# Kernel optimization log

Hardware: AMD Instinct MI355X
Metric: run time of the kernel (lower is better)

## Reference

```python
import jax, jax.numpy as jnp
import numpy as np

N_NODES = 2048
N_EDGES = 32768
DIM = 256
HEADS = 4

PARAM_SHAPES = {
    'Wq': (DIM, DIM), 'bq': (DIM,), 'Wk': (DIM, DIM), 'bk': (DIM,),
    'Wv': (DIM, DIM), 'bv': (DIM,), 'Wo': (DIM, DIM), 'bo': (DIM,),
    'gd_W1': (4, 3), 'gd_b1': (3,), 'gd_W2': (3, HEADS), 'gd_b2': (HEADS,),
    'tw_W1': (2 * DIM, DIM), 'tw_b1': (DIM,), 'tw_W2': (DIM, DIM), 'tw_b2': (DIM,),
    'ne_W1': (4 * DIM, 2 * DIM), 'ne_b1': (2 * DIM,), 'ne_W2': (2 * DIM, DIM), 'ne_b2': (DIM,),
    'att_W1': (2 * DIM // HEADS, 2 * DIM // HEADS), 'att_b1': (2 * DIM // HEADS,),
    'att_W2': (DIM // HEADS, 2 * DIM // HEADS), 'att_b2': (DIM // HEADS,),
    'pe_W': (DIM, DIM), 'pe_b': (DIM,), 'pq_W': (DIM, DIM), 'pq_b': (DIM,),
    'pv_W': (DIM, DIM), 'pv_b': (DIM,),
    'pr_W1': (2 * DIM, 2 * DIM), 'pr_b1': (2 * DIM,), 'pr_W2': (2 * DIM, DIM), 'pr_b2': (DIM,),
}


def _lin(x, W, b):
    return x @ W + b


def _mlp2(x, W1, b1, W2, b2):  # Linear-ReLU-Linear (build_mlp, on_last=False)
    return _lin(jnp.maximum(_lin(x, W1, b1), 0.0), W2, b2)


def setup_inputs() -> dict:
    key = jax.random.key(0)
    ks = iter(jax.random.split(key, 64))
    rng = np.random.default_rng(0)
    half = N_EDGES // 2
    s = rng.integers(0, N_NODES, half)
    d = rng.integers(0, N_NODES, half)
    # reciprocal edge pairs so the reverse-edge lookup path is exercised
    edge_index = jnp.asarray(np.stack([np.concatenate([s, d]), np.concatenate([d, s])]), dtype=jnp.int32)
    inp = {
        'node_f': jax.random.normal(next(ks), (N_NODES, DIM), jnp.float32),
        'edge_f': jax.random.normal(next(ks), (N_EDGES, DIM), jnp.float32),
        'coords': jax.random.normal(next(ks), (N_NODES, 3), jnp.float32),
        'edge_index': edge_index,
        'num_heads': HEADS,
    }
    for name, shp in PARAM_SHAPES.items():
        inp[name] = jax.random.normal(next(ks), shp, jnp.float32) * 0.02
    return inp


def _forward(node_f, edge_f, coords, edge_index, num_heads,
             Wq, bq, Wk, bk, Wv, bv, Wo, bo,
             gd_W1, gd_b1, gd_W2, gd_b2,
             tw_W1, tw_b1, tw_W2, tw_b2,
             ne_W1, ne_b1, ne_W2, ne_b2,
             att_W1, att_b1, att_W2, att_b2,
             pe_W, pe_b, pq_W, pq_b, pv_W, pv_b,
             pr_W1, pr_b1, pr_W2, pr_b2):
    N, Dn = node_f.shape
    E, De = edge_f.shape
    H = num_heads
    dh = Wq.shape[1] // H
    src, dst = edge_index[0], edge_index[1]

    # --- NodeUpdate: distance-aware MHSA over all node pairs (batch=1) ---
    q = _lin(node_f, Wq, bq).reshape(N, H, dh)
    k = _lin(node_f, Wk, bk).reshape(N, H, dh)
    v = _lin(node_f, Wv, bv).reshape(N, H, dh)
    diff = coords[:, None, :] - coords[None, :, :]  # [N,N,3]
    sq = jnp.sum(diff * diff, axis=-1, keepdims=True)
    dist = jnp.where(sq > 0, jnp.sqrt(jnp.where(sq > 0, sq, 1.0)), 0.0)
    dmask = _mlp2(jnp.concatenate([diff, dist], -1), gd_W1, gd_b1, gd_W2, gd_b2)  # [N,N,H]
    scores = jnp.einsum('nhd,mhd->hnm', q, k) / float(dh) ** 0.5 + dmask.transpose(2, 0, 1)
    attn = jax.nn.softmax(scores, axis=-1)
    mhsa = _lin(jnp.einsum('hnm,mhd->nhd', attn, v).reshape(N, H * dh), Wo, bo)

    # --- TwinningEdgeAttention: per-node mean of outgoing / incoming edge feats ---
    ones = jnp.ones((E,), edge_f.dtype)
    cnt_s = jnp.maximum(jax.ops.segment_sum(ones, src, num_segments=N), 1.0)
    cnt_d = jnp.maximum(jax.ops.segment_sum(ones, dst, num_segments=N), 1.0)
    sub_mean = jax.ops.segment_sum(edge_f, src, num_segments=N) / cnt_s[:, None]
    obj_mean = jax.ops.segment_sum(edge_f, dst, num_segments=N) / cnt_d[:, None]
    edge_att = jax.nn.sigmoid(_mlp2(jnp.concatenate([sub_mean, obj_mean], -1), tw_W1, tw_b1, tw_W2, tw_b2))
    node_out = jnp.maximum(mhsa, 0.0) * edge_att  # [N, Dn]

    # --- GraphEdgeAttenNetwork ---
    x_i = node_f[src]
    x_j = node_f[dst]
    # reverse-edge matching (vectorized replacement of the python double loop)
    table = jnp.zeros((N * N,), jnp.int32).at[src * N + dst].set(jnp.arange(E, dtype=jnp.int32) + 1)
    rev = table[dst * N + src]
    rev_feat = jnp.where((rev > 0)[:, None], edge_f[jnp.maximum(rev - 1, 0)], 0.0)
    edge_out = _mlp2(jnp.concatenate([x_i, edge_f, rev_feat, x_j], -1), ne_W1, ne_b1, ne_W2, ne_b2)

    value = _lin(x_j, pv_W, pv_b)  # [E, Da]
    query = _lin(x_i, pq_W, pq_b).reshape(E, Dn // H, H)
    edgep = _lin(edge_f, pe_W, pe_b).reshape(E, De // H, H)
    qe = jnp.concatenate([query, edgep], axis=1)  # [E, d_n+d_e, H]
    # conv1d(kernel=1) MLP over channel axis, ReLU between layers
    h = jnp.maximum(jnp.einsum('ech,oc->eoh', qe, att_W1) + att_b1[None, :, None], 0.0)
    prob = jax.nn.softmax(jnp.einsum('ech,oc->eoh', h, att_W2) + att_b2[None, :, None], axis=1)  # [E, d_o, H]
    msg = prob.reshape(E, -1) * value
    agg = jax.ops.segment_max(msg, src, num_segments=N)
    agg = jnp.where(jnp.isfinite(agg), agg, 0.0)  # empty segments -> 0 (torch scatter_max fill)
    xx = _mlp2(jnp.concatenate([node_f, agg], -1), pr_W1, pr_b1, pr_W2, pr_b2)
    return node_out, edge_out, xx


def reference(node_f, edge_f, coords, edge_index, num_heads,
              Wq, bq, Wk, bk, Wv, bv, Wo, bo,
              gd_W1, gd_b1, gd_W2, gd_b2,
              tw_W1, tw_b1, tw_W2, tw_b2,
              ne_W1, ne_b1, ne_W2, ne_b2,
              att_W1, att_b1, att_W2, att_b2,
              pe_W, pe_b, pq_W, pq_b, pv_W, pv_b,
              pr_W1, pr_b1, pr_W2, pr_b2):
    return _forward(node_f, edge_f, coords, edge_index, num_heads,
                    Wq, bq, Wk, bk, Wv, bv, Wo, bo,
                    gd_W1, gd_b1, gd_W2, gd_b2,
                    tw_W1, tw_b1, tw_W2, tw_b2,
                    ne_W1, ne_b1, ne_W2, ne_b2,
                    att_W1, att_b1, att_W2, att_b2,
                    pe_W, pe_b, pq_W, pq_b, pv_W, pv_b,
                    pr_W1, pr_b1, pr_W2, pr_b2)
```

## Files before the change

### kernel.cpp

```cpp
#include <hip/hip_runtime.h>

#define NN 2048
#define NE 32768
#define DIM 256
#define NH 4

typedef unsigned short u16;
typedef __attribute__((ext_vector_type(4))) unsigned short u16x4;
typedef __attribute__((ext_vector_type(8))) short bf16x8;
typedef __attribute__((ext_vector_type(4))) float f32x4;

typedef __attribute__((address_space(1))) const unsigned int g_as1;
typedef __attribute__((address_space(3))) unsigned int l_as3;

__device__ __forceinline__ void gload16(const u16* g, u16* l) {
  __builtin_amdgcn_global_load_lds((g_as1*)g, (l_as3*)l, 16, 0, 0);
}

__device__ __forceinline__ u16 f2bf(float f) {
  unsigned u = __float_as_uint(f);
  unsigned r = u + 0x7FFFu + ((u >> 16) & 1u);
  return (u16)(r >> 16);
}
__device__ __forceinline__ float bf2f(u16 b) {
  return __uint_as_float(((unsigned)b) << 16);
}

struct GB { const u16* A; const int* idx; long ld; long aoffz; };

template<int BNF, int EPI>
__global__ __launch_bounds__(256) void gemm_bf(
    GB ga, const u16* __restrict__ Bt, long bld, long boffz,
    const float* __restrict__ bias, void* __restrict__ Cp, long ldc, long coffz,
    int K, float scale)
{
  __shared__ u16 As[128 * 64];
  __shared__ u16 Bs[32 * BNF * 64];

  const int tid = threadIdx.x;
  const int wid = tid >> 6, lane = tid & 63;
  const int bz = blockIdx.z;
  const int m0 = blockIdx.y * 128;
  const int n0 = blockIdx.x * (32 * BNF);
  const int wr = wid >> 1, wc = wid & 1;
  const int l15 = lane & 15, l4 = lane >> 4;

  const u16* asrc[4];
  #pragma unroll
  for (int c = 0; c < 4; ++c) {
    int rl = c*32 + wid*8 + (lane >> 3);
    int row = ga.idx ? ga.idx[m0 + rl] : (m0 + rl);
    int c16s = (lane & 7) ^ (rl & 7);
    asrc[c] = ga.A + ga.aoffz * bz + (long)row * ga.ld + c16s * 8;
  }
  const u16* bsrc[BNF];
  #pragma unroll
  for (int c = 0; c < BNF; ++c) {
    int rl = c*32 + wid*8 + (lane >> 3);
    int c16s = (lane & 7) ^ (rl & 7);
    bsrc[c] = Bt + boffz * bz + (long)(n0 + rl) * bld + c16s * 8;
  }

  f32x4 acc[4][BNF] = {};

  for (int k0 = 0; k0 < K; k0 += 64) {
    #pragma unroll
    for (int c = 0; c < 4; ++c)
      gload16(asrc[c] + k0, &As[(c*32 + wid*8) * 64]);
    #pragma unroll
    for (int c = 0; c < BNF; ++c)
      gload16(bsrc[c] + k0, &Bs[(c*32 + wid*8) * 64]);
    __syncthreads();

    #pragma unroll
    for (int kk = 0; kk < 2; ++kk) {
      bf16x8 af[4], bfr[BNF];
      #pragma unroll
      for (int i = 0; i < 4; ++i) {
        int r = wr*64 + i*16 + l15;
        af[i] = *(const bf16x8*)&As[r*64 + (((kk*4 + l4) ^ (r & 7)) * 8)];
      }
      #pragma unroll
      for (int j = 0; j < BNF; ++j) {
        int r = wc*(16*BNF) + j*16 + l15;
        bfr[j] = *(const bf16x8*)&Bs[r*64 + (((kk*4 + l4) ^ (r & 7)) * 8)];
      }
      #pragma unroll
      for (int i = 0; i < 4; ++i)
        #pragma unroll
        for (int j = 0; j < BNF; ++j)
          acc[i][j] = __builtin_amdgcn_mfma_f32_16x16x32_bf16(af[i], bfr[j], acc[i][j], 0, 0, 0);
    }
    __syncthreads();
  }

  #pragma unroll
  for (int j = 0; j < BNF; ++j) {
    const int col = n0 + wc*(16*BNF) + j*16 + l15;
    const float bb = bias ? bias[col] : 0.f;
    #pragma unroll
    for (int i = 0; i < 4; ++i) {
      #pragma unroll
      for (int r = 0; r < 4; ++r) {
        const int m = m0 + wr*64 + i*16 + l4*4 + r;
        float v = acc[i][j][r] * scale + bb;
        if constexpr (EPI == 1) v = fmaxf(v, 0.f);
        if constexpr (EPI == 2) v = 1.f / (1.f + expf(-v));
        if constexpr (EPI == 0 || EPI == 2)
          ((float*)Cp)[coffz*bz + (long)m*ldc + col] = v;
        else if constexpr (EPI == 4)
          ((u16*)Cp)[((long)(col & 3) * NE + m) * ldc + (col >> 2) + coffz] = f2bf(v);
        else if constexpr (EPI == 6)
          ((float*)Cp)[(long)m*256 + (col & 3)*64 + (col >> 2)] = v;
        else if constexpr (EPI == 7)
          ((u16*)Cp)[((long)(col & 3) * NN + m) * ldc + (col >> 2) + coffz] = f2bf(v);
        else
          ((u16*)Cp)[coffz*bz + (long)m*ldc + col] = f2bf(v);
      }
    }
  }
}

__global__ __launch_bounds__(256) void flash_k(
    const u16* __restrict__ qkv,
    const u16* __restrict__ vT,
    const float4* __restrict__ pk,
    const float* __restrict__ gW1, const float* __restrict__ gb1,
    const float* __restrict__ gW2, const float* __restrict__ gb2,
    float* __restrict__ Op,
    float2* __restrict__ ml)
{
  __shared__ u16 Qls[64*64];
  __shared__ u16 Kls[128*64];
  __shared__ u16 Vls[2][64*64];
  __shared__ u16 Pls[4][16*128];

  const int tid = threadIdx.x, wid = tid >> 6, lane = tid & 63;
  const int h  = blockIdx.x & 3;
  const int m0 = (blockIdx.x >> 2) * 64;
  const int part = blockIdx.y;
  const int l15 = lane & 15, l4 = lane >> 4;
  const int rl8 = wid*8 + (lane >> 3);
  const int c8  = lane & 7;

  #pragma unroll
  for (int c = 0; c < 2; ++c) {
    int r = c*32 + rl8;
    gload16(qkv + (long)(m0 + r)*768 + h*64 + ((c8 ^ (r & 7))*8), &Qls[(c*32 + wid*8)*64]);
  }
  __syncthreads();
  bf16x8 qf[2];
  {
    int r = wid*16 + l15;
    qf[0] = *(const bf16x8*)&Qls[r*64 + (((0*4 + l4) ^ (r & 7))*8)];
    qf[1] = *(const bf16x8*)&Qls[r*64 + (((1*4 + l4) ^ (r & 7))*8)];
  }

  const float b10 = gb1[0], b11 = gb1[1], b12 = gb1[2];
  const float w30 = gW1[9], w31 = gW1[10], w32 = gW1[11];
  const float w20 = gW2[0*4+h], w21 = gW2[1*4+h], w22 = gW2[2*4+h];
  const float b2h = gb2[h];
  float4 rp0[4], rp1[4];
  #pragma unroll
  for (int r = 0; r < 4; ++r) {
    int qrow = m0 + wid*16 + l4*4 + r;
    rp0[r] = pk[qrow*2]; rp1[r] = pk[qrow*2 + 1];
  }

  float mrun[4] = {-1e30f, -1e30f, -1e30f, -1e30f};
  float lrun[4] = {};
  f32x4 pa[4] = {};

  for (int t = 0; t < 4; ++t) {
    const int n0 = part*512 + t*128;
    #pragma unroll
    for (int c = 0; c < 4; ++c) {
      int r = c*32 + rl8;
      gload16(qkv + (long)(n0 + r)*768 + 256 + h*64 + ((c8 ^ (r & 7))*8),
              &Kls[(c*32 + wid*8)*64]);
    }
    #pragma unroll
    for (int hh = 0; hh < 2; ++hh)
      #pragma unroll
      for (int c = 0; c < 2; ++c) {
        int r = c*32 + rl8;
        gload16(vT + (long)(h*64 + r)*NN + n0 + hh*64 + ((c8 ^ (r & 7))*8),
                &Vls[hh][(c*32 + wid*8)*64]);
      }
    __syncthreads();

    f32x4 sa[8] = {};
    #pragma unroll
    for (int kk = 0; kk < 2; ++kk) {
      #pragma unroll
      for (int j = 0; j < 8; ++j) {
        int r = j*16 + l15;
        bf16x8 bf = *(const bf16x8*)&Kls[r*64 + (((kk*4 + l4) ^ (r & 7))*8)];
        sa[j] = __builtin_amdgcn_mfma_f32_16x16x32_bf16(qf[kk], bf, sa[j], 0, 0, 0);
      }
    }

    float rowmx[4] = {-1e30f, -1e30f, -1e30f, -1e30f};
    #pragma unroll
    for (int j = 0; j < 8; ++j) {
      int n = n0 + j*16 + l15;
      float4 cp0 = pk[n*2], cp1 = pk[n*2 + 1];
      #pragma unroll
      for (int r = 0; r < 4; ++r) {
        float dot = rp0[r].x*cp0.x + rp0[r].y*cp0.y + rp0[r].z*cp0.z;
        float sq = rp0[r].w + cp0.w - 2.f*dot;
        float dist = sq > 0.f ? sq * __frsqrt_rn(sq) : 0.f;
        float h0 = fmaxf(b10 + rp1[r].x - cp1.x + dist*w30, 0.f);
        float h1 = fmaxf(b11 + rp1[r].y - cp1.y + dist*w31, 0.f);
        float h2 = fmaxf(b12 + rp1[r].z - cp1.z + dist*w32, 0.f);
        float s = sa[j][r]*0.125f + b2h + h0*w20 + h1*w21 + h2*w22;
        sa[j][r] = s;
        rowmx[r] = fmaxf(rowmx[r], s);
      }
    }
    #pragma unroll
    for (int w = 1; w < 16; w <<= 1)
      #pragma unroll
      for (int r = 0; r < 4; ++r)
        rowmx[r] = fmaxf(rowmx[r], __shfl_xor(rowmx[r], w));

    float fac[4], rs[4] = {};
    #pragma unroll
    for (int r = 0; r < 4; ++r) {
      float mnew = fmaxf(mrun[r], rowmx[r]);
      fac[r] = __expf(mrun[r] - mnew);
      mrun[r] = mnew;
    }
    #pragma unroll
    for (int j = 0; j < 8; ++j)
      #pragma unroll
      for (int r = 0; r < 4; ++r) {
        float p = __expf(sa[j][r] - mrun[r]);
        sa[j][r] = p;
        rs[r] += p;
      }
    #pragma unroll
    for (int w = 1; w < 16; w <<= 1)
      #pragma unroll
      for (int r = 0; r < 4; ++r)
        rs[r] += __shfl_xor(rs[r], w);
    #pragma unroll
    for (int r = 0; r < 4; ++r) lrun[r] = lrun[r]*fac[r] + rs[r];
    #pragma unroll
    for (int j2 = 0; j2 < 4; ++j2)
      #pragma unroll
      for (int r = 0; r < 4; ++r)
        pa[j2][r] *= fac[r];

    #pragma unroll
    for (int j = 0; j < 8; ++j)
      #pragma unroll
      for (int r = 0; r < 4; ++r) {
        int qr = l4*4 + r, n = j*16 + l15;
        Pls[wid][qr*128 + (((n >> 3) ^ (qr & 7))*8) + (n & 7)] = f2bf(sa[j][r]);
      }
    #pragma unroll
    for (int ks = 0; ks < 4; ++ks) {
      bf16x8 paf = *(const bf16x8*)&Pls[wid][l15*128 + (((ks*4 + l4) ^ (l15 & 7))*8)];
      #pragma unroll
      for (int j2 = 0; j2 < 4; ++j2) {
        int r = j2*16 + l15;
        bf16x8 vf = *(const bf16x8*)&Vls[ks >> 1][r*64 + ((((ks & 1)*4 + l4) ^ (r & 7))*8)];
        pa[j2] = __builtin_amdgcn_mfma_f32_16x16x32_bf16(paf, vf, pa[j2], 0, 0, 0);
      }
    }
    __syncthreads();
  }

  #pragma unroll
  for (int j2 = 0; j2 < 4; ++j2)
    #pragma unroll
    for (int r = 0; r < 4; ++r) {
      int m = m0 + wid*16 + l4*4 + r;
      Op[((long)part*NN + m)*256 + h*64 + j2*16 + l15] = pa[j2][r];
    }
  if (l15 == 0) {
    #pragma unroll
    for (int r = 0; r < 4; ++r) {
      int m = m0 + wid*16 + l4*4 + r;
      ml[((long)part*NN + m)*4 + h] = make_float2(mrun[r], lrun[r]);
    }
  }
}

__global__ __launch_bounds__(256) void comb_k(const float* __restrict__ Op,
    const float2* __restrict__ ml, u16* __restrict__ attn) {
  int n = blockIdx.x, t = threadIdx.x, h = t >> 6;
  float m[4], l[4];
  #pragma unroll
  for (int p = 0; p < 4; ++p) { float2 v = ml[((long)p*NN + n)*4 + h]; m[p] = v.x; l[p] = v.y; }
  float M = fmaxf(fmaxf(m[0], m[1]), fmaxf(m[2], m[3]));
  float L = 0.f, o = 0.f;
  #pragma unroll
  for (int p = 0; p < 4; ++p) {
    float w = __expf(m[p] - M);
    L += w * l[p];
    o += w * Op[((long)p*NN + n)*256 + t];
  }
  attn[(long)n*256 + t] = f2bf(o / L);
}

__global__ __launch_bounds__(64) void attedge_k(
    const u16* __restrict__ qN, const u16* __restrict__ ep,
    const float* __restrict__ valNp, const int* __restrict__ ei,
    const u16* __restrict__ W1, const float* __restrict__ b1,
    const u16* __restrict__ W2, const float* __restrict__ b2,
    float* __restrict__ msgP)
{
  __shared__ u16 As[32*128];
  const int lane = threadIdx.x;
  const int h = blockIdx.y;
  const int e0 = blockIdx.x * 32;
  const int l15 = lane & 15, l4 = lane >> 4;

  #pragma unroll
  for (int p = 0; p < 8; ++p) {
    int R0 = p*4;
    int r  = R0 + (lane >> 4);
    int cd = lane & 15;
    int cs = ((cd & 7) ^ (r & 7)) | (cd & 8);
    const u16* src = (cs < 8)
        ? qN + ((long)h*NN + ei[e0 + r])*64 + cs*8
        : ep + ((long)h*NE + e0 + r)*64 + (cs & 7)*8;
    gload16(src, &As[R0*128]);
  }
  __syncthreads();

  f32x4 acc1[2][8] = {};
  #pragma unroll
  for (int kk = 0; kk < 4; ++kk) {
    bf16x8 af[2], bfr[8];
    #pragma unroll
    for (int i = 0; i < 2; ++i) {
      int rA = i*16 + l15;
      int cg = kk*4 + l4;
      int cd = ((cg & 7) ^ (rA & 7)) | (cg & 8);
      af[i] = *(const bf16x8*)&As[rA*128 + cd*8];
    }
    #pragma unroll
    for (int j = 0; j < 8; ++j)
      bfr[j] = *(const bf16x8*)&W1[(long)(j*16 + l15)*128 + kk*32 + l4*8];
    #pragma unroll
    for (int i = 0; i < 2; ++i)
      #pragma unroll
      for (int j = 0; j < 8; ++j)
        acc1[i][j] = __builtin_amdgcn_mfma_f32_16x16x32_bf16(af[i], bfr[j], acc1[i][j], 0, 0, 0);
  }
  __syncthreads();
  #pragma unroll
  for (int i = 0; i < 2; ++i)
    #pragma unroll
    for (int j = 0; j < 8; ++j) {
      int n = j*16 + l15;
      float bb = b1[n];
      #pragma unroll
      for (int r = 0; r < 4; ++r) {
        int m = i*16 + l4*4 + r;
        int cg = n >> 3;
        int cd = ((cg & 7) ^ (m & 7)) | (cg & 8);
        As[m*128 + cd*8 + (n & 7)] = f2bf(fmaxf(acc1[i][j][r] + bb, 0.f));
      }
    }
  __syncthreads();

  f32x4 acc2[2][4] = {};
  #pragma unroll
  for (int kk = 0; kk < 4; ++kk) {
    bf16x8 af[2], bfr[4];
    #pragma unroll
    for (int i = 0; i < 2; ++i) {
      int rA = i*16 + l15;
      int cg = kk*4 + l4;
      int cd = ((cg & 7) ^ (rA & 7)) | (cg & 8);
      af[i] = *(const bf16x8*)&As[rA*128 + cd*8];
    }
    #pragma unroll
    for (int j = 0; j < 4; ++j)
      bfr[j] = *(const bf16x8*)&W2[(long)(j*16 + l15)*128 + kk*32 + l4*8];
    #pragma unroll
    for (int i = 0; i < 2; ++i)
      #pragma unroll
      for (int j = 0; j < 4; ++j)
        acc2[i][j] = __builtin_amdgcn_mfma_f32_16x16x32_bf16(af[i], bfr[j], acc2[i][j], 0, 0, 0);
  }

  #pragma unroll
  for (int i = 0; i < 2; ++i) {
    float mx[4] = {-1e30f,-1e30f,-1e30f,-1e30f};
    #pragma unroll
    for (int j = 0; j < 4; ++j) {
      float bb = b2[j*16 + l15];
      #pragma unroll
      for (int r = 0; r < 4; ++r) {
        acc2[i][j][r] += bb;
        mx[r] = fmaxf(mx[r], acc2[i][j][r]);
      }
    }
    #pragma unroll
    for (int w = 1; w < 16; w <<= 1)
      #pragma unroll
      for (int r = 0; r < 4; ++r) mx[r] = fmaxf(mx[r], __shfl_xor(mx[r], w));
    float sum[4] = {};
    #pragma unroll
    for (int j = 0; j < 4; ++j)
      #pragma unroll
      for (int r = 0; r < 4; ++r) {
        float p = __expf(acc2[i][j][r] - mx[r]);
        acc2[i][j][r] = p; sum[r] += p;
      }
    #pragma unroll
    for (int w = 1; w < 16; w <<= 1)
      #pragma unroll
      for (int r = 0; r < 4; ++r) sum[r] += __shfl_xor(sum[r], w);
    #pragma unroll
    for (int r = 0; r < 4; ++r) {
      int m = i*16 + l4*4 + r;
      int e = e0 + m;
      int dst = ei[NE + e];
      float inv = 1.f / sum[r];
      #pragma unroll
      for (int j = 0; j < 4; ++j) {
        int o = j*16 + l15;
        float v = valNp[(long)dst*256 + h*64 + o];
        msgP[(long)e*256 + h*64 + o] = acc2[i][j][r] * inv * v;
      }
    }
  }
}

__global__ __launch_bounds__(256) void gemm_ne(
    const u16* __restrict__ nbf, const u16* __restrict__ ebf, const u16* __restrict__ zbuf,
    const int* __restrict__ ei, const int* __restrict__ rev,
    const u16* __restrict__ Bt, const float* __restrict__ bias, u16* __restrict__ C)
{
  __shared__ u16 As[128 * 64];
  __shared__ u16 Bs[128 * 64];
  const int tid = threadIdx.x, wid = tid >> 6, lane = tid & 63;
  const int lin = blockIdx.y * 4 + blockIdx.x;
  const int xcd = lin & 7, seq = lin >> 3;
  const int m0 = (xcd*32 + (seq >> 2)) * 128;
  const int n0 = (seq & 3) * 128;
  const int wr = wid >> 1, wc = wid & 1, l15 = lane & 15, l4 = lane >> 4;

  const u16* bsrc[4];
  #pragma unroll
  for (int c = 0; c < 4; ++c) {
    int rl = c*32 + wid*8 + (lane >> 3);
    int c16s = (lane & 7) ^ (rl & 7);
    bsrc[c] = Bt + (long)(n0 + rl) * 1024 + c16s * 8;
  }

  f32x4 acc[4][4] = {};

  #pragma unroll
  for (int seg = 0; seg < 4; ++seg) {
    const u16* asrc[4];
    #pragma unroll
    for (int c = 0; c < 4; ++c) {
      int rl = c*32 + wid*8 + (lane >> 3);
      int m = m0 + rl;
      int c16s = (lane & 7) ^ (rl & 7);
      const u16* base; long row;
      if (seg == 0)      { base = nbf; row = ei[m]; }
      else if (seg == 1) { base = ebf; row = m; }
      else if (seg == 2) { int r = rev[m]; base = (r >= 0) ? ebf : zbuf; row = (r >= 0) ? r : 0; }
      else               { base = nbf; row = ei[NE + m]; }
      asrc[c] = base + row * 256 + c16s * 8;
    }
    #pragma unroll
    for (int kt = 0; kt < 4; ++kt) {
      #pragma unroll
      for (int c = 0; c < 4; ++c)
        gload16(asrc[c] + kt*64, &As[(c*32 + wid*8) * 64]);
      #pragma unroll
      for (int c = 0; c < 4; ++c)
        gload16(bsrc[c] + seg*256 + kt*64, &Bs[(c*32 + wid*8) * 64]);
      __syncthreads();
      #pragma unroll
      for (int kk = 0; kk < 2; ++kk) {
        bf16x8 af[4], bfr[4];
        #pragma unroll
        for (int i = 0; i < 4; ++i) {
          int r = wr*64 + i*16 + l15;
          af[i] = *(const bf16x8*)&As[r*64 + (((kk*4 + l4) ^ (r & 7)) * 8)];
        }
        #pragma unroll
        for (int j = 0; j < 4; ++j) {
          int r = wc*64 + j*16 + l15;
          bfr[j] = *(const bf16x8*)&Bs[r*64 + (((kk*4 + l4) ^ (r & 7)) * 8)];
        }
        #pragma unroll
        for (int i = 0; i < 4; ++i)
          #pragma unroll
          for (int j = 0; j < 4; ++j)
            acc[i][j] = __builtin_amdgcn_mfma_f32_16x16x32_bf16(af[i], bfr[j], acc[i][j], 0, 0, 0);
      }
      __syncthreads();
    }
  }

  #pragma unroll
  for (int j = 0; j < 4; ++j) {
    const int col = n0 + wc*64 + j*16 + l15;
    const float bb = bias[col];
    #pragma unroll
    for (int i = 0; i < 4; ++i) {
      #pragma unroll
      for (int r = 0; r < 4; ++r) {
        const int m = m0 + wr*64 + i*16 + l4*4 + r;
        C[(long)m*512 + col] = f2bf(fmaxf(acc[i][j][r] + bb, 0.f));
      }
    }
  }
}

struct PrepEnt { const float* src; void* dst; int K; int N; int ntiles; int op; };
struct PrepDesc { PrepEnt e[24]; int n; };

__global__ __launch_bounds__(256) void wprep_k(PrepDesc d) {
  __shared__ float t[32][33];
  int b = blockIdx.x;
  int ei = 0;
  while (ei < d.n && b >= d.e[ei].ntiles) { b -= d.e[ei].ntiles; ++ei; }
  if (ei >= d.n) return;
  PrepEnt E = d.e[ei];
  int tid = threadIdx.x;
  if (E.op == 0) {
    int kt = E.K >> 5;
    int bk = (b % kt) * 32, bn = (b / kt) * 32;
    int tx = tid & 31, ty = tid >> 5;
    #pragma unroll
    for (int i = ty; i < 32; i += 8) t[i][tx] = E.src[(long)(bk + i) * E.N + bn + tx];
    __syncthreads();
    u16* dst = (u16*)E.dst;
    #pragma unroll
    for (int i = ty; i < 32; i += 8) dst[(long)(bn + i) * E.K + bk + tx] = f2bf(t[tx][i]);
  } else if (E.op == 1) {
    long i = (long)b * 256 + tid;
    long n4 = ((long)E.K * E.N) >> 2;
    if (i < n4) {
      float4 v = ((const float4*)E.src)[i];
      u16x4 o = { f2bf(v.x), f2bf(v.y), f2bf(v.z), f2bf(v.w) };
      ((u16x4*)E.dst)[i] = o;
    }
  } else {
    int i = b * 256 + tid;
    if (i < E.N) ((float*)E.dst)[i] = E.src[i];
  }
}

__global__ void geo_k(const float* __restrict__ C3, const float* __restrict__ gW1,
                      float* __restrict__ geo) {
  int n = blockIdx.x * 256 + threadIdx.x;
  if (n >= NN) return;
  float cx = C3[3*n], cy = C3[3*n+1], cz = C3[3*n+2];
  float s = cx*cx + cy*cy + cz*cz;
  float a0 = cx*gW1[0] + cy*gW1[3] + cz*gW1[6];
  float a1 = cx*gW1[1] + cy*gW1[4] + cz*gW1[7];
  float a2 = cx*gW1[2] + cy*gW1[5] + cz*gW1[8];
  float4* g = (float4*)(geo + (long)n*8);
  g[0] = make_float4(cx, cy, cz, s);
  g[1] = make_float4(a0, a1, a2, 0.f);
}

__global__ __launch_bounds__(256) void transb_k(const u16* __restrict__ src,
                                                u16* __restrict__ dst) {
  __shared__ u16 t[32][34];
  int bm = blockIdx.x * 32, bc = blockIdx.y * 32;
  int tx = threadIdx.x & 31, ty = threadIdx.x >> 5;
  #pragma unroll
  for (int i = ty; i < 32; i += 8) t[i][tx] = src[(long)(bm+i)*768 + 512 + bc + tx];
  __syncthreads();
  #pragma unroll
  for (int i = ty; i < 32; i += 8) dst[(long)(bc+i)*NN + bm + tx] = t[tx][i];
}

__global__ __launch_bounds__(256) void seg_sum_k(const float* __restrict__ ef,
    const int* __restrict__ ei, float* sub, float* obj, float* cs, float* cd) {
  int e = blockIdx.x * 4 + (threadIdx.x >> 6);
  int lane = threadIdx.x & 63;
  int s = ei[e], d = ei[NE + e];
  const float* row = ef + (long)e * DIM;
  #pragma unroll
  for (int c = 0; c < 4; ++c) {
    float v = row[lane + c*64];
    atomicAdd(&sub[(long)s*DIM + lane + c*64], v);
    atomicAdd(&obj[(long)d*DIM + lane + c*64], v);
  }
  if (lane == 0) { atomicAdd(&cs[s], 1.f); atomicAdd(&cd[d], 1.f); }
}

__global__ void pack_tw_k(const float* __restrict__ sub, const float* __restrict__ obj,
    const float* __restrict__ cs, const float* __restrict__ cd, u16* __restrict__ twA) {
  int n = blockIdx.x, t = threadIdx.x;
  int seg = t >> 6, c = (t & 63) * 4;
  float sc = seg ? 1.f / fmaxf(cd[n], 1.f) : 1.f / fmaxf(cs[n], 1.f);
  float4 v = *(const float4*)((seg ? obj : sub) + (long)n * DIM + c);
  u16x4 o = { f2bf(v.x*sc), f2bf(v.y*sc), f2bf(v.z*sc), f2bf(v.w*sc) };
  *(u16x4*)&twA[(long)n*512 + seg*256 + c] = o;
}

__global__ void pack_pr_k(const float* __restrict__ nf, const float* __restrict__ agg,
                          u16* __restrict__ prA) {
  int n = blockIdx.x, t = threadIdx.x;
  int seg = t >> 6, c = (t & 63) * 4;
  float4 v = *(const float4*)((seg ? agg : nf) + (long)n * DIM + c);
  u16x4 o = { f2bf(v.x), f2bf(v.y), f2bf(v.z), f2bf(v.w) };
  *(u16x4*)&prA[(long)n*512 + seg*256 + c] = o;
}

__global__ void node_out_k(const float* mh, const float* ea, float* out) {
  long i = (long)blockIdx.x * 256 + threadIdx.x;
  out[i] = fmaxf(mh[i], 0.f) * ea[i];
}

__global__ void scat_k(const int* ei, int* tbl) {
  int e = blockIdx.x * 256 + threadIdx.x;
  atomicMax(&tbl[(long)ei[e] * NN + ei[NE + e]], e + 1);
}

__global__ void rev_k(const int* ei, const int* tbl, int* rev) {
  int e = blockIdx.x * 256 + threadIdx.x;
  rev[e] = tbl[(long)ei[NE + e] * NN + ei[e]] - 1;
}

__global__ __launch_bounds__(256) void scan_k(const float* __restrict__ cs,
    int* __restrict__ start, int* __restrict__ cursor) {
  __shared__ int part[256];
  int t = threadIdx.x;
  int loc[8]; int s = 0;
  #pragma unroll
  for (int i = 0; i < 8; ++i) { int v = (int)cs[t*8 + i]; loc[i] = s; s += v; }
  part[t] = s;
  __syncthreads();
  if (t == 0) { int a = 0; for (int i = 0; i < 256; ++i) { int v = part[i]; part[i] = a; a += v; } }
  __syncthreads();
  int base = part[t];
  #pragma unroll
  for (int i = 0; i < 8; ++i) { start[t*8+i] = base + loc[i]; cursor[t*8+i] = base + loc[i]; }
  if (t == 255) start[2048] = base + s;
}

__global__ void scatter_k(const int* __restrict__ ei, int* __restrict__ cursor,
                          int* __restrict__ eids) {
  int e = blockIdx.x * 256 + threadIdx.x;
  int pos = atomicAdd(&cursor[ei[e]], 1);
  eids[pos] = e;
}

__global__ __launch_bounds__(256) void agg_k(const int* __restrict__ start,
    const int* __restrict__ eids, const float* __restrict__ msgP, float* __restrict__ aggf) {
  int n = blockIdx.x, t = threadIdx.x;
  int b = start[n], e_ = start[n+1];
  float mx = -1e30f;
  for (int i = b; i < e_; ++i) {
    int e = eids[i];
    mx = fmaxf(mx, msgP[(long)e*256 + t]);
  }
  int c = (t & 63) * 4 + (t >> 6);
  aggf[(long)n*256 + c] = (e_ > b) ? mx : 0.f;
}

static GB gb(const u16* A, const int* idx, long ld, long aoffz) {
  GB g; g.A = A; g.idx = idx; g.ld = ld; g.aoffz = aoffz; return g;
}

extern "C" void kernel_launch(void* const* d_in, const int* in_sizes, int n_in,
                              void* d_out, int out_size, void* d_ws, size_t ws_size,
                              hipStream_t stream) {
  (void)in_sizes; (void)n_in; (void)out_size; (void)ws_size;

  const float* node_f = (const float*)d_in[0];
  const float* edge_f = (const float*)d_in[1];
  const float* coords = (const float*)d_in[2];
  const int*   ei     = (const int*)d_in[3];
  const float* Wq = (const float*)d_in[5];  const float* bq = (const float*)d_in[6];
  const float* Wk = (const float*)d_in[7];  const float* bk = (const float*)d_in[8];
  const float* Wv = (const float*)d_in[9];  const float* bv = (const float*)d_in[10];
  const float* Wo = (const float*)d_in[11]; const float* bo = (const float*)d_in[12];
  const float* gd_W1 = (const float*)d_in[13]; const float* gd_b1 = (const float*)d_in[14];
  const float* gd_W2 = (const float*)d_in[15]; const float* gd_b2 = (const float*)d_in[16];
  const float* tw_W1 = (const float*)d_in[17]; const float* tw_b1 = (const float*)d_in[18];
  const float* tw_W2 = (const float*)d_in[19]; const float* tw_b2 = (const float*)d_in[20];
  const float* ne_W1 = (const float*)d_in[21]; const float* ne_b1 = (const float*)d_in[22];
  const float* ne_W2 = (const float*)d_in[23]; const float* ne_b2 = (const float*)d_in[24];
  const float* att_W1 = (const float*)d_in[25]; const float* att_b1 = (const float*)d_in[26];
  const float* att_W2 = (const float*)d_in[27]; const float* att_b2 = (const float*)d_in[28];
  const float* pe_W = (const float*)d_in[29]; const float* pe_b = (const float*)d_in[30];
  const float* pq_W = (const float*)d_in[31]; const float* pq_b = (const float*)d_in[32];
  const float* pv_W = (const float*)d_in[33]; const float* pv_b = (const float*)d_in[34];
  const float* pr_W1 = (const float*)d_in[35]; const float* pr_b1 = (const float*)d_in[36];
  const float* pr_W2 = (const float*)d_in[37]; const float* pr_b2 = (const float*)d_in[38];

  char* WB = (char*)d_ws;
  float* out = (float*)d_out;
  float* out_node = out;
  float* out_edge = out + (long)NN*DIM;
  float* out_xx   = out + (long)NN*DIM + (long)NE*DIM;

  const long sz_R1 = 4L*NN*NN*4;
  const long sz_R2 = 4L*NN*NN*2;
  const long sz_R3 = 4L*NE*128*2;
  const long R1 = 0, R2 = R1 + sz_R1, R3 = R2 + sz_R2;

  float*  Opart = (float*)(WB + R1);
  float2* mlbuf = (float2*)(WB + R1 + 4L*NN*256*4);
  float*  msgP  = (float*)(WB + R1);
  u16*   nehid  = (u16*)(WB + R2);
  int*   tbl    = (int*)(WB + R3);
  u16*   ep     = (u16*)(WB + R3);
  u16*   edge_bf= (u16*)(WB + R3 + (long)NN*NN*4);

  long cur = R3 + sz_R3;
  auto alloc = [&](long bytes) { long o = cur; cur += (bytes + 255) & ~255L; return o; };

  long o_sub = alloc(2L*NN*DIM*4);
  float* sub = (float*)(WB + o_sub);
  float* obj = sub + (long)NN*DIM;
  u16* qkv_bf  = (u16*)sub;
  u16* vT      = (u16*)obj;
  u16* attn_bf = vT + (long)NN*DIM;

  long o_cs  = alloc(2L*NN*4);
  float* cs = (float*)(WB + o_cs); float* cd = cs + NN;
  long o_mh  = alloc((long)NN*DIM*4);  float* mhsa = (float*)(WB + o_mh);
  long o_ea  = alloc((long)NN*DIM*4);  float* eatt = (float*)(WB + o_ea);
  long o_ag  = alloc((long)NN*DIM*4);  float* aggf = (float*)(WB + o_ag);
  long o_rv  = alloc((long)NE*4);      int* rev = (int*)(WB + o_rv);
  long o_st  = alloc((NN+1)*4);        int* startp = (int*)(WB + o_st);
  long o_cu  = alloc(NN*4);            int* cursor = (int*)(WB + o_cu);
  long o_eid = alloc((long)NE*4);      int* eids = (int*)(WB + o_eid);
  long o_zb  = alloc(1024);            u16* zbuf = (u16*)(WB + o_zb);
  long o_geo = alloc((long)NN*8*4);    float* geo = (float*)(WB + o_geo);
  long o_nbf = alloc((long)NN*DIM*2);  u16* node_bf = (u16*)(WB + o_nbf);
  long o_twA = alloc((long)NN*512*2);  u16* twA = (u16*)(WB + o_twA);
  long o_twh = alloc((long)NN*DIM*2);  u16* twh = (u16*)(WB + o_twh);
  long o_prA = alloc((long)NN*512*2);  u16* prA = (u16*)(WB + o_prA);
  long o_prh = alloc((long)NN*512*2);  u16* prh = (u16*)(WB + o_prh);
  long o_qN  = alloc(4L*NN*64*2);      u16* qN = (u16*)(WB + o_qN);
  long o_vN  = alloc((long)NN*DIM*4);  float* valN = (float*)(WB + o_vN);

  u16* qkv_t = (u16*)(WB + alloc(3L*DIM*DIM*2));
  u16* Wo_t  = (u16*)(WB + alloc(DIM*DIM*2));
  u16* tw1_t = (u16*)(WB + alloc(DIM*512*2));
  u16* tw2_t = (u16*)(WB + alloc(DIM*DIM*2));
  u16* ne1_t = (u16*)(WB + alloc(512L*1024*2));
  u16* ne2_t = (u16*)(WB + alloc(DIM*512*2));
  u16* pe_t  = (u16*)(WB + alloc(DIM*DIM*2));
  u16* pq_t  = (u16*)(WB + alloc(DIM*DIM*2));
  u16* pv_t  = (u16*)(WB + alloc(DIM*DIM*2));
  u16* pr1_t = (u16*)(WB + alloc(512L*512*2));
  u16* pr2_t = (u16*)(WB + alloc(DIM*512*2));
  u16* a1_bf = (u16*)(WB + alloc(128*128*2));
  u16* a2_bf = (u16*)(WB + alloc(64*128*2));
  float* qkvb = (float*)(WB + alloc(768*4));

  hipMemsetAsync(sub, 0, 2L*NN*DIM*4, stream);
  hipMemsetAsync(cs, 0, 2L*NN*4, stream);
  hipMemsetAsync(tbl, 0, (long)NN*NN*4, stream);
  hipMemsetAsync(zbuf, 0, 1024, stream);

  PrepDesc pd{}; int ne_ = 0; int tot = 0;
  auto addT = [&](const float* s, u16* d, int K, int N) {
    pd.e[ne_] = { s, d, K, N, (K/32)*(N/32), 0 }; tot += pd.e[ne_].ntiles; ++ne_;
  };
  auto addC = [&](const float* s, u16* d, long elems) {
    int nt = (int)((elems/4 + 255) / 256);
    pd.e[ne_] = { s, d, 1, (int)elems, nt, 1 }; tot += nt; ++ne_;
  };
  auto addB = [&](const float* s, float* d, int n) {
    pd.e[ne_] = { s, d, 1, n, (n + 255)/256, 2 }; tot += pd.e[ne_].ntiles; ++ne_;
  };
  addT(Wq, qkv_t,               DIM, DIM);
  addT(Wk, qkv_t + DIM*DIM,     DIM, DIM);
  addT(Wv, qkv_t + 2*DIM*DIM,   DIM, DIM);
  addT(Wo, Wo_t, DIM, DIM);
  addT(tw_W1, tw1_t, 512, DIM);
  addT(tw_W2, tw2_t, DIM, DIM);
  addT(ne_W1, ne1_t, 1024, 512);
  addT(ne_W2, ne2_t, 512, DIM);
  addT(pe_W, pe_t, DIM, DIM);
  addT(pq_W, pq_t, DIM, DIM);
  addT(pv_W, pv_t, DIM, DIM);
  addT(pr_W1, pr1_t, 512, 512);
  addT(pr_W2, pr2_t, 512, DIM);
  addC(att_W1, a1_bf, 128*128);
  addC(att_W2, a2_bf, 64*128);
  addC(node_f, node_bf, (long)NN*DIM);
  addC(edge_f, edge_bf, (long)NE*DIM);
  addB(bq, qkvb, 256); addB(bk, qkvb + 256, 256); addB(bv, qkvb + 512, 256);
  pd.n = ne_;
  wprep_k<<<tot, 256, 0, stream>>>(pd);
  geo_k<<<NN/256, 256, 0, stream>>>(coords, gd_W1, geo);

  seg_sum_k<<<NE/4, 256, 0, stream>>>(edge_f, ei, sub, obj, cs, cd);
  scan_k<<<1, 256, 0, stream>>>(cs, startp, cursor);
  scatter_k<<<NE/256, 256, 0, stream>>>(ei, cursor, eids);
  pack_tw_k<<<NN, 128, 0, stream>>>(sub, obj, cs, cd, twA);
  gemm_bf<4,1><<<dim3(2,16,1), 256, 0, stream>>>(gb(twA, nullptr, 512, 0), tw1_t, 512, 0,
      tw_b1, twh, DIM, 0, 512, 1.f);
  gemm_bf<4,2><<<dim3(2,16,1), 256, 0, stream>>>(gb(twh, nullptr, DIM, 0), tw2_t, DIM, 0,
      tw_b2, eatt, DIM, 0, DIM, 1.f);

  gemm_bf<4,5><<<dim3(6,16,1), 256, 0, stream>>>(gb(node_bf, nullptr, DIM, 0), qkv_t, DIM, 0,
      qkvb, qkv_bf, 768, 0, DIM, 1.f);
  transb_k<<<dim3(64,8), 256, 0, stream>>>(qkv_bf, vT);
  flash_k<<<dim3(128,4), 256, 0, stream>>>(qkv_bf, vT, (const float4*)geo,
      gd_W1, gd_b1, gd_W2, gd_b2, Opart, mlbuf);
  comb_k<<<NN, 256, 0, stream>>>(Opart, mlbuf, attn_bf);
  gemm_bf<4,0><<<dim3(2,16,1), 256, 0, stream>>>(gb(attn_bf, nullptr, DIM, 0), Wo_t, DIM, 0,
      bo, mhsa, DIM, 0, DIM, 1.f);
  node_out_k<<<NN, 256, 0, stream>>>(mhsa, eatt, out_node);

  scat_k<<<NE/256, 256, 0, stream>>>(ei, tbl);
  rev_k<<<NE/256, 256, 0, stream>>>(ei, tbl, rev);
  gemm_ne<<<dim3(4,256,1), 256, 0, stream>>>(node_bf, edge_bf, zbuf, ei, rev,
      ne1_t, ne_b1, nehid);
  gemm_bf<4,0><<<dim3(2,256,1), 256, 0, stream>>>(gb(nehid, nullptr, 512, 0), ne2_t, 512, 0,
      ne_b2, out_edge, DIM, 0, 512, 1.f);

  gemm_bf<4,6><<<dim3(2,16,1), 256, 0, stream>>>(gb(node_bf, nullptr, DIM, 0), pv_t, DIM, 0,
      pv_b, valN, DIM, 0, DIM, 1.f);
  gemm_bf<4,7><<<dim3(2,16,1), 256, 0, stream>>>(gb(node_bf, nullptr, DIM, 0), pq_t, DIM, 0,
      pq_b, qN, 64, 0, DIM, 1.f);
  gemm_bf<4,4><<<dim3(2,256,1), 256, 0, stream>>>(gb(edge_bf, nullptr, DIM, 0), pe_t, DIM, 0,
      pe_b, ep, 64, 0, DIM, 1.f);
  attedge_k<<<dim3(NE/32, NH), 64, 0, stream>>>(qN, ep, valN, ei,
      a1_bf, att_b1, a2_bf, att_b2, msgP);
  agg_k<<<NN, 256, 0, stream>>>(startp, eids, msgP, aggf);

  pack_pr_k<<<NN, 128, 0, stream>>>(node_f, aggf, prA);
  gemm_bf<4,1><<<dim3(4,16,1), 256, 0, stream>>>(gb(prA, nullptr, 512, 0), pr1_t, 512, 0,
      pr_b1, prh, 512, 0, 512, 1.f);
  gemm_bf<4,0><<<dim3(2,16,1), 256, 0, stream>>>(gb(prh, nullptr, 512, 0), pr2_t, 512, 0,
      pr_b2, out_xx, DIM, 0, 512, 1.f);
}
```

Measured before the change: 434.2 us.

## Double-buffer gemm_ne, widen flash split, fuse pv/pq GEMMs and pr packing

The edge-node GEMM now double-buffers its A/B LDS tiles, precomputes all gather pointers up front and uses explicit vmcnt waits so loads overlap MFMA work. Flash attention splits the key range into 8 parts instead of 4, and the combine kernel merges 8 partials. The pv and pq node projections become one GEMM with a split epilogue. agg_k writes bf16 directly into the pr input buffer, and the node_f half is converted inside the prep kernel, which removes the pack kernel. attedge_k processes 64 edges per block to reuse its weight fragments, at the cost of more registers and LDS.

```diff
diff --git a/kernel.cpp b/kernel.cpp
--- a/kernel.cpp
+++ b/kernel.cpp
@@ -21,9 +21,6 @@
   unsigned u = __float_as_uint(f);
   unsigned r = u + 0x7FFFu + ((u >> 16) & 1u);
   return (u16)(r >> 16);
-}
-__device__ __forceinline__ float bf2f(u16 b) {
-  return __uint_as_float(((unsigned)b) << 16);
 }
 
 struct GB { const u16* A; const int* idx; long ld; long aoffz; };
@@ -110,10 +107,15 @@
           ((float*)Cp)[coffz*bz + (long)m*ldc + col] = v;
         else if constexpr (EPI == 4)
           ((u16*)Cp)[((long)(col & 3) * NE + m) * ldc + (col >> 2) + coffz] = f2bf(v);
-        else if constexpr (EPI == 6)
-          ((float*)Cp)[(long)m*256 + (col & 3)*64 + (col >> 2)] = v;
-        else if constexpr (EPI == 7)
-          ((u16*)Cp)[((long)(col & 3) * NN + m) * ldc + (col >> 2) + coffz] = f2bf(v);
+        else if constexpr (EPI == 8) {
+          if (col < 256)
+            ((float*)Cp)[(long)m*256 + (col & 3)*64 + (col >> 2)] = v;
+          else {
+            u16* qb = (u16*)((float*)Cp + (long)NN*256);
+            int c2 = col - 256;
+            qb[((long)(c2 & 3)*NN + m)*64 + (c2 >> 2)] = f2bf(v);
+          }
+        }
         else
           ((u16*)Cp)[coffz*bz + (long)m*ldc + col] = f2bf(v);
       }
@@ -171,8 +173,8 @@
   float lrun[4] = {};
   f32x4 pa[4] = {};
 
-  for (int t = 0; t < 4; ++t) {
-    const int n0 = part*512 + t*128;
+  for (int t = 0; t < 2; ++t) {
+    const int n0 = part*256 + t*128;
     #pragma unroll
     for (int c = 0; c < 4; ++c) {
       int r = c*32 + rl8;
@@ -291,13 +293,15 @@
 __global__ __launch_bounds__(256) void comb_k(const float* __restrict__ Op,
     const float2* __restrict__ ml, u16* __restrict__ attn) {
   int n = blockIdx.x, t = threadIdx.x, h = t >> 6;
-  float m[4], l[4];
-  #pragma unroll
-  for (int p = 0; p < 4; ++p) { float2 v = ml[((long)p*NN + n)*4 + h]; m[p] = v.x; l[p] = v.y; }
-  float M = fmaxf(fmaxf(m[0], m[1]), fmaxf(m[2], m[3]));
+  float m[8], l[8];
+  #pragma unroll
+  for (int p = 0; p < 8; ++p) { float2 v = ml[((long)p*NN + n)*4 + h]; m[p] = v.x; l[p] = v.y; }
+  float M = m[0];
+  #pragma unroll
+  for (int p = 1; p < 8; ++p) M = fmaxf(M, m[p]);
   float L = 0.f, o = 0.f;
   #pragma unroll
-  for (int p = 0; p < 4; ++p) {
+  for (int p = 0; p < 8; ++p) {
     float w = __expf(m[p] - M);
     L += w * l[p];
     o += w * Op[((long)p*NN + n)*256 + t];
@@ -312,14 +316,14 @@
     const u16* __restrict__ W2, const float* __restrict__ b2,
     float* __restrict__ msgP)
 {
-  __shared__ u16 As[32*128];
+  __shared__ u16 As[64*128];
   const int lane = threadIdx.x;
   const int h = blockIdx.y;
-  const int e0 = blockIdx.x * 32;
+  const int e0 = blockIdx.x * 64;
   const int l15 = lane & 15, l4 = lane >> 4;
 
   #pragma unroll
-  for (int p = 0; p < 8; ++p) {
+  for (int p = 0; p < 16; ++p) {
     int R0 = p*4;
     int r  = R0 + (lane >> 4);
     int cd = lane & 15;
@@ -331,29 +335,27 @@
   }
   __syncthreads();
 
-  f32x4 acc1[2][8] = {};
+  f32x4 acc1[4][8] = {};
   #pragma unroll
   for (int kk = 0; kk < 4; ++kk) {
-    bf16x8 af[2], bfr[8];
-    #pragma unroll
-    for (int i = 0; i < 2; ++i) {
+    bf16x8 bfr[8];
+    #pragma unroll
+    for (int j = 0; j < 8; ++j)
+      bfr[j] = *(const bf16x8*)&W1[(long)(j*16 + l15)*128 + kk*32 + l4*8];
+    #pragma unroll
+    for (int i = 0; i < 4; ++i) {
       int rA = i*16 + l15;
       int cg = kk*4 + l4;
       int cd = ((cg & 7) ^ (rA & 7)) | (cg & 8);
-      af[i] = *(const bf16x8*)&As[rA*128 + cd*8];
-    }
-    #pragma unroll
-    for (int j = 0; j < 8; ++j)
-      bfr[j] = *(const bf16x8*)&W1[(long)(j*16 + l15)*128 + kk*32 + l4*8];
-    #pragma unroll
-    for (int i = 0; i < 2; ++i)
+      bf16x8 af = *(const bf16x8*)&As[rA*128 + cd*8];
       #pragma unroll
       for (int j = 0; j < 8; ++j)
-        acc1[i][j] = __builtin_amdgcn_mfma_f32_16x16x32_bf16(af[i], bfr[j], acc1[i][j], 0, 0, 0);
+        acc1[i][j] = __builtin_amdgcn_mfma_f32_16x16x32_bf16(af, bfr[j], acc1[i][j], 0, 0, 0);
+    }
   }
   __syncthreads();
   #pragma unroll
-  for (int i = 0; i < 2; ++i)
+  for (int i = 0; i < 4; ++i)
     #pragma unroll
     for (int j = 0; j < 8; ++j) {
       int n = j*16 + l15;
@@ -368,29 +370,27 @@
     }
   __syncthreads();
 
-  f32x4 acc2[2][4] = {};
+  f32x4 acc2[4][4] = {};
   #pragma unroll
   for (int kk = 0; kk < 4; ++kk) {
-    bf16x8 af[2], bfr[4];
-    #pragma unroll
-    for (int i = 0; i < 2; ++i) {
+    bf16x8 bfr[4];
+    #pragma unroll
+    for (int j = 0; j < 4; ++j)
+      bfr[j] = *(const bf16x8*)&W2[(long)(j*16 + l15)*128 + kk*32 + l4*8];
+    #pragma unroll
+    for (int i = 0; i < 4; ++i) {
       int rA = i*16 + l15;
       int cg = kk*4 + l4;
       int cd = ((cg & 7) ^ (rA & 7)) | (cg & 8);
-      af[i] = *(const bf16x8*)&As[rA*128 + cd*8];
-    }
-    #pragma unroll
-    for (int j = 0; j < 4; ++j)
-      bfr[j] = *(const bf16x8*)&W2[(long)(j*16 + l15)*128 + kk*32 + l4*8];
-    #pragma unroll
-    for (int i = 0; i < 2; ++i)
+      bf16x8 af = *(const bf16x8*)&As[rA*128 + cd*8];
       #pragma unroll
       for (int j = 0; j < 4; ++j)
-        acc2[i][j] = __builtin_amdgcn_mfma_f32_16x16x32_bf16(af[i], bfr[j], acc2[i][j], 0, 0, 0);
-  }
-
-  #pragma unroll
-  for (int i = 0; i < 2; ++i) {
+        acc2[i][j] = __builtin_amdgcn_mfma_f32_16x16x32_bf16(af, bfr[j], acc2[i][j], 0, 0, 0);
+    }
+  }
+
+  #pragma unroll
+  for (int i = 0; i < 4; ++i) {
     float mx[4] = {-1e30f,-1e30f,-1e30f,-1e30f};
     #pragma unroll
     for (int j = 0; j < 4; ++j) {
@@ -438,8 +438,8 @@
     const int* __restrict__ ei, const int* __restrict__ rev,
     const u16* __restrict__ Bt, const float* __restrict__ bias, u16* __restrict__ C)
 {
-  __shared__ u16 As[128 * 64];
-  __shared__ u16 Bs[128 * 64];
+  __shared__ u16 As[2][128 * 64];
+  __shared__ u16 Bs[2][128 * 64];
   const int tid = threadIdx.x, wid = tid >> 6, lane = tid & 63;
   const int lin = blockIdx.y * 4 + blockIdx.x;
   const int xcd = lin & 7, seq = lin >> 3;
@@ -447,6 +447,18 @@
   const int n0 = (seq & 3) * 128;
   const int wr = wid >> 1, wc = wid & 1, l15 = lane & 15, l4 = lane >> 4;
 
+  const u16* asrc[4][4];
+  #pragma unroll
+  for (int c = 0; c < 4; ++c) {
+    int rl = c*32 + wid*8 + (lane >> 3);
+    int m = m0 + rl;
+    int c16s = ((lane & 7) ^ (rl & 7)) * 8;
+    int si = ei[m], di = ei[NE + m], rv = rev[m];
+    asrc[0][c] = nbf + (long)si * 256 + c16s;
+    asrc[1][c] = ebf + (long)m * 256 + c16s;
+    asrc[2][c] = (rv >= 0 ? ebf + (long)rv * 256 : zbuf) + c16s;
+    asrc[3][c] = nbf + (long)di * 256 + c16s;
+  }
   const u16* bsrc[4];
   #pragma unroll
   for (int c = 0; c < 4; ++c) {
@@ -457,52 +469,51 @@
 
   f32x4 acc[4][4] = {};
 
-  #pragma unroll
-  for (int seg = 0; seg < 4; ++seg) {
-    const u16* asrc[4];
-    #pragma unroll
-    for (int c = 0; c < 4; ++c) {
-      int rl = c*32 + wid*8 + (lane >> 3);
-      int m = m0 + rl;
-      int c16s = (lane & 7) ^ (rl & 7);
-      const u16* base; long row;
-      if (seg == 0)      { base = nbf; row = ei[m]; }
-      else if (seg == 1) { base = ebf; row = m; }
-      else if (seg == 2) { int r = rev[m]; base = (r >= 0) ? ebf : zbuf; row = (r >= 0) ? r : 0; }
-      else               { base = nbf; row = ei[NE + m]; }
-      asrc[c] = base + row * 256 + c16s * 8;
-    }
-    #pragma unroll
-    for (int kt = 0; kt < 4; ++kt) {
-      #pragma unroll
-      for (int c = 0; c < 4; ++c)
-        gload16(asrc[c] + kt*64, &As[(c*32 + wid*8) * 64]);
-      #pragma unroll
-      for (int c = 0; c < 4; ++c)
-        gload16(bsrc[c] + seg*256 + kt*64, &Bs[(c*32 + wid*8) * 64]);
-      __syncthreads();
-      #pragma unroll
-      for (int kk = 0; kk < 2; ++kk) {
-        bf16x8 af[4], bfr[4];
+#define NE_STAGE(BUF, IT) do {                                                  \
+    const int seg_ = (IT) >> 2, kt_ = (IT) & 3;                                 \
+    _Pragma("unroll")                                                           \
+    for (int c = 0; c < 4; ++c)                                                 \
+      gload16(asrc[seg_][c] + kt_*64, &As[BUF][(c*32 + wid*8) * 64]);           \
+    _Pragma("unroll")                                                           \
+    for (int c = 0; c < 4; ++c)                                                 \
+      gload16(bsrc[c] + seg_*256 + kt_*64, &Bs[BUF][(c*32 + wid*8) * 64]);      \
+  } while (0)
+
+  NE_STAGE(0, 0);
+  #pragma unroll
+  for (int it = 0; it < 16; ++it) {
+    const int b = it & 1;
+    if (it < 15) {
+      NE_STAGE(b ^ 1, it + 1);
+      asm volatile("s_waitcnt vmcnt(8)" ::: "memory");
+    } else {
+      asm volatile("s_waitcnt vmcnt(0)" ::: "memory");
+    }
+    __builtin_amdgcn_s_barrier();
+    asm volatile("" ::: "memory");
+    #pragma unroll
+    for (int kk = 0; kk < 2; ++kk) {
+      bf16x8 af[4], bfr[4];
+      #pragma unroll
+      for (int i = 0; i < 4; ++i) {
+        int r = wr*64 + i*16 + l15;
+        af[i] = *(const bf16x8*)&As[b][r*64 + (((kk*4 + l4) ^ (r & 7)) * 8)];
+      }
+      #pragma unroll
+      for (int j = 0; j < 4; ++j) {
+        int r = wc*64 + j*16 + l15;
+        bfr[j] = *(const bf16x8*)&Bs[b][r*64 + (((kk*4 + l4) ^ (r & 7)) * 8)];
+      }
+      #pragma unroll
+      for (int i = 0; i < 4; ++i)
         #pragma unroll
-        for (int i = 0; i < 4; ++i) {
-          int r = wr*64 + i*16 + l15;
-          af[i] = *(const bf16x8*)&As[r*64 + (((kk*4 + l4) ^ (r & 7)) * 8)];
-        }
-        #pragma unroll
-        for (int j = 0; j < 4; ++j) {
-          int r = wc*64 + j*16 + l15;
-          bfr[j] = *(const bf16x8*)&Bs[r*64 + (((kk*4 + l4) ^ (r & 7)) * 8)];
-        }
-        #pragma unroll
-        for (int i = 0; i < 4; ++i)
-          #pragma unroll
-          for (int j = 0; j < 4; ++j)
-            acc[i][j] = __builtin_amdgcn_mfma_f32_16x16x32_bf16(af[i], bfr[j], acc[i][j], 0, 0, 0);
-      }
-      __syncthreads();
-    }
-  }
+        for (int j = 0; j < 4; ++j)
+          acc[i][j] = __builtin_amdgcn_mfma_f32_16x16x32_bf16(af[i], bfr[j], acc[i][j], 0, 0, 0);
+    }
+    asm volatile("" ::: "memory");
+    __builtin_amdgcn_s_barrier();
+  }
+#undef NE_STAGE
 
   #pragma unroll
   for (int j = 0; j < 4; ++j) {
@@ -548,6 +559,16 @@
       u16x4 o = { f2bf(v.x), f2bf(v.y), f2bf(v.z), f2bf(v.w) };
       ((u16x4*)E.dst)[i] = o;
     }
+  } else if (E.op == 3) {
+    long i = (long)b * 256 + tid;
+    long n4 = ((long)E.K * E.N) >> 2;
+    if (i < n4) {
+      float4 v = ((const float4*)E.src)[i];
+      long row = i >> 6;
+      long col = (i & 63) * 4;
+      u16x4 o = { f2bf(v.x), f2bf(v.y), f2bf(v.z), f2bf(v.w) };
+      *(u16x4*)((u16*)E.dst + row*512 + col) = o;
+    }
   } else {
     int i = b * 256 + tid;
     if (i < E.N) ((float*)E.dst)[i] = E.src[i];
@@ -605,15 +626,6 @@
   *(u16x4*)&twA[(long)n*512 + seg*256 + c] = o;
 }
 
-__global__ void pack_pr_k(const float* __restrict__ nf, const float* __restrict__ agg,
-                          u16* __restrict__ prA) {
-  int n = blockIdx.x, t = threadIdx.x;
-  int seg = t >> 6, c = (t & 63) * 4;
-  float4 v = *(const float4*)((seg ? agg : nf) + (long)n * DIM + c);
-  u16x4 o = { f2bf(v.x), f2bf(v.y), f2bf(v.z), f2bf(v.w) };
-  *(u16x4*)&prA[(long)n*512 + seg*256 + c] = o;
-}
-
 __global__ void node_out_k(const float* mh, const float* ea, float* out) {
   long i = (long)blockIdx.x * 256 + threadIdx.x;
   out[i] = fmaxf(mh[i], 0.f) * ea[i];
@@ -654,7 +666,7 @@
 }
 
 __global__ __launch_bounds__(256) void agg_k(const int* __restrict__ start,
-    const int* __restrict__ eids, const float* __restrict__ msgP, float* __restrict__ aggf) {
+    const int* __restrict__ eids, const float* __restrict__ msgP, u16* __restrict__ prA) {
   int n = blockIdx.x, t = threadIdx.x;
   int b = start[n], e_ = start[n+1];
   float mx = -1e30f;
@@ -663,7 +675,7 @@
     mx = fmaxf(mx, msgP[(long)e*256 + t]);
   }
   int c = (t & 63) * 4 + (t >> 6);
-  aggf[(long)n*256 + c] = (e_ > b) ? mx : 0.f;
+  prA[(long)n*512 + 256 + c] = f2bf((e_ > b) ? mx : 0.f);
 }
 
 static GB gb(const u16* A, const int* idx, long ld, long aoffz) {
@@ -709,7 +721,7 @@
   const long R1 = 0, R2 = R1 + sz_R1, R3 = R2 + sz_R2;
 
   float*  Opart = (float*)(WB + R1);
-  float2* mlbuf = (float2*)(WB + R1 + 4L*NN*256*4);
+  float2* mlbuf = (float2*)(WB + R1 + 8L*NN*256*4);
   float*  msgP  = (float*)(WB + R1);
   u16*   nehid  = (u16*)(WB + R2);
   int*   tbl    = (int*)(WB + R3);
@@ -730,7 +742,6 @@
   float* cs = (float*)(WB + o_cs); float* cd = cs + NN;
   long o_mh  = alloc((long)NN*DIM*4);  float* mhsa = (float*)(WB + o_mh);
   long o_ea  = alloc((long)NN*DIM*4);  float* eatt = (float*)(WB + o_ea);
-  long o_ag  = alloc((long)NN*DIM*4);  float* aggf = (float*)(WB + o_ag);
   long o_rv  = alloc((long)NE*4);      int* rev = (int*)(WB + o_rv);
   long o_st  = alloc((NN+1)*4);        int* startp = (int*)(WB + o_st);
   long o_cu  = alloc(NN*4);            int* cursor = (int*)(WB + o_cu);
@@ -742,8 +753,9 @@
   long o_twh = alloc((long)NN*DIM*2);  u16* twh = (u16*)(WB + o_twh);
   long o_prA = alloc((long)NN*512*2);  u16* prA = (u16*)(WB + o_prA);
   long o_prh = alloc((long)NN*512*2);  u16* prh = (u16*)(WB + o_prh);
-  long o_qN  = alloc(4L*NN*64*2);      u16* qN = (u16*)(WB + o_qN);
-  long o_vN  = alloc((long)NN*DIM*4);  float* valN = (float*)(WB + o_vN);
+  long o_vN  = alloc((long)NN*256*4 + 4L*NN*64*2);
+  float* valN = (float*)(WB + o_vN);
+  u16*   qN   = (u16*)(valN + (long)NN*256);
 
   u16* qkv_t = (u16*)(WB + alloc(3L*DIM*DIM*2));
   u16* Wo_t  = (u16*)(WB + alloc(DIM*DIM*2));
@@ -752,13 +764,13 @@
   u16* ne1_t = (u16*)(WB + alloc(512L*1024*2));
   u16* ne2_t = (u16*)(WB + alloc(DIM*512*2));
   u16* pe_t  = (u16*)(WB + alloc(DIM*DIM*2));
-  u16* pq_t  = (u16*)(WB + alloc(DIM*DIM*2));
-  u16* pv_t  = (u16*)(WB + alloc(DIM*DIM*2));
+  u16* pvq_t = (u16*)(WB + alloc(2L*DIM*DIM*2));
   u16* pr1_t = (u16*)(WB + alloc(512L*512*2));
   u16* pr2_t = (u16*)(WB + alloc(DIM*512*2));
   u16* a1_bf = (u16*)(WB + alloc(128*128*2));
   u16* a2_bf = (u16*)(WB + alloc(64*128*2));
   float* qkvb = (float*)(WB + alloc(768*4));
+  float* pvqb = (float*)(WB + alloc(512*4));
 
   hipMemsetAsync(sub, 0, 2L*NN*DIM*4, stream);
   hipMemsetAsync(cs, 0, 2L*NN*4, stream);
@@ -785,8 +797,8 @@
   addT(ne_W1, ne1_t, 1024, 512);
   addT(ne_W2, ne2_t, 512, DIM);
   addT(pe_W, pe_t, DIM, DIM);
-  addT(pq_W, pq_t, DIM, DIM);
-  addT(pv_W, pv_t, DIM, DIM);
+  addT(pv_W, pvq_t,             DIM, DIM);
+  addT(pq_W, pvq_t + DIM*DIM,   DIM, DIM);
   addT(pr_W1, pr1_t, 512, 512);
   addT(pr_W2, pr2_t, 512, DIM);
   addC(att_W1, a1_bf, 128*128);
@@ -794,6 +806,9 @@
   addC(node_f, node_bf, (long)NN*DIM);
   addC(edge_f, edge_bf, (long)NE*DIM);
   addB(bq, qkvb, 256); addB(bk, qkvb + 256, 256); addB(bv, qkvb + 512, 256);
+  addB(pv_b, pvqb, 256); addB(pq_b, pvqb + 256, 256);
+  pd.e[ne_] = { node_f, prA, NN, 256, (int)(((long)NN*256/4 + 255)/256), 3 };
+  tot += pd.e[ne_].ntiles; ++ne_;
   pd.n = ne_;
   wprep_k<<<tot, 256, 0, stream>>>(pd);
   geo_k<<<NN/256, 256, 0, stream>>>(coords, gd_W1, geo);
@@ -810,7 +825,7 @@
   gemm_bf<4,5><<<dim3(6,16,1), 256, 0, stream>>>(gb(node_bf, nullptr, DIM, 0), qkv_t, DIM, 0,
       qkvb, qkv_bf, 768, 0, DIM, 1.f);
   transb_k<<<dim3(64,8), 256, 0, stream>>>(qkv_bf, vT);
-  flash_k<<<dim3(128,4), 256, 0, stream>>>(qkv_bf, vT, (const float4*)geo,
+  flash_k<<<dim3(128,8), 256, 0, stream>>>(qkv_bf, vT, (const float4*)geo,
       gd_W1, gd_b1, gd_W2, gd_b2, Opart, mlbuf);
   comb_k<<<NN, 256, 0, stream>>>(Opart, mlbuf, attn_bf);
   gemm_bf<4,0><<<dim3(2,16,1), 256, 0, stream>>>(gb(attn_bf, nullptr, DIM, 0), Wo_t, DIM, 0,
@@ -824,17 +839,14 @@
   gemm_bf<4,0><<<dim3(2,256,1), 256, 0, stream>>>(gb(nehid, nullptr, 512, 0), ne2_t, 512, 0,
       ne_b2, out_edge, DIM, 0, 512, 1.f);
 
-  gemm_bf<4,6><<<dim3(2,16,1), 256, 0, stream>>>(gb(node_bf, nullptr, DIM, 0), pv_t, DIM, 0,
-      pv_b, valN, DIM, 0, DIM, 1.f);
-  gemm_bf<4,7><<<dim3(2,16,1), 256, 0, stream>>>(gb(node_bf, nullptr, DIM, 0), pq_t, DIM, 0,
-      pq_b, qN, 64, 0, DIM, 1.f);
+  gemm_bf<4,8><<<dim3(4,16,1), 256, 0, stream>>>(gb(node_bf, nullptr, DIM, 0), pvq_t, DIM, 0,
+      pvqb, valN, 256, 0, DIM, 1.f);
   gemm_bf<4,4><<<dim3(2,256,1), 256, 0, stream>>>(gb(edge_bf, nullptr, DIM, 0), pe_t, DIM, 0,
       pe_b, ep, 64, 0, DIM, 1.f);
-  attedge_k<<<dim3(NE/32, NH), 64, 0, stream>>>(qN, ep, valN, ei,
+  attedge_k<<<dim3(NE/64, NH), 64, 0, stream>>>(qN, ep, valN, ei,
       a1_bf, att_b1, a2_bf, att_b2, msgP);
-  agg_k<<<NN, 256, 0, stream>>>(startp, eids, msgP, aggf);
-
-  pack_pr_k<<<NN, 128, 0, stream>>>(node_f, aggf, prA);
+  agg_k<<<NN, 256, 0, stream>>>(startp, eids, msgP, prA);
+
   gemm_bf<4,1><<<dim3(4,16,1), 256, 0, stream>>>(gb(prA, nullptr, 512, 0), pr1_t, 512, 0,
       pr_b1, prh, 512, 0, 512, 1.f);
   gemm_bf<4,0><<<dim3(2,16,1), 256, 0, stream>>>(gb(prh, nullptr, 512, 0), pr2_t, 512, 0,
```

Result: slower. 476.2 us (+9.7%).
